# Optimization experiments

Measured on AMD Instinct MI355X. Metric: run time of the kernel, lower is better.

The kernel has to match this reference:

```python
import jax, jax.numpy as jnp
import numpy as np

HEADS = 8
DIM_HEAD = 64
WINDOW = 256
CAUSAL = True


def _sliding_window_mask(seq_len: int, window: int, causal: bool) -> jnp.ndarray:
    i = jnp.arange(seq_len)[:, None]
    j = jnp.arange(seq_len)[None, :]
    # attend iff i - window + 1 <= j <= i + window - 1 (end_pos exclusive)
    mask = (j >= i - window + 1) & (j <= i + window - 1)
    if causal:
        mask = mask & (j <= i)
    return mask  # (S, S) bool


def setup_inputs() -> dict:
    key = jax.random.key(0)
    k1, k2, k3 = jax.random.split(key, 3)
    dim = 512
    inner = HEADS * DIM_HEAD
    x = jax.random.normal(k1, (2, 2048, dim), dtype=jnp.float32)
    W_qkv = jax.random.normal(k2, (dim, 3 * inner), dtype=jnp.float32) * 0.02
    W_out = jax.random.normal(k3, (inner, dim), dtype=jnp.float32) * 0.02
    return {"x": x, "W_qkv": W_qkv, "W_out": W_out}


def reference(x, W_qkv, W_out):
    B, S, D = x.shape
    H, Dh = HEADS, DIM_HEAD
    scale = Dh ** (-0.5)
    qkv = x @ W_qkv  # (B, S, 3*H*Dh)
    q, k, v = jnp.split(qkv, 3, axis=-1)
    q = q.reshape(B, S, H, Dh).transpose(0, 2, 1, 3)  # (B, H, S, Dh)
    k = k.reshape(B, S, H, Dh).transpose(0, 2, 1, 3)
    v = v.reshape(B, S, H, Dh).transpose(0, 2, 1, 3)
    scores = jnp.einsum('bhid,bhjd->bhij', q, k) * scale
    mask = _sliding_window_mask(S, WINDOW, CAUSAL)
    mask_value = -jnp.finfo(scores.dtype).max
    scores = jnp.where(mask[None, None, :, :], scores, mask_value)
    attn = jax.nn.softmax(scores, axis=-1)  # (B, H, S, S)
    out = jnp.einsum('bhij,bhjd->bhid', attn, v)
    out = out.transpose(0, 2, 1, 3).reshape(B, S, H * Dh)
    out = out @ W_out  # (B, S, D)
    return (out, attn)
```

## Files before the change

### kernel.cpp

```cpp
#include <hip/hip_runtime.h>
#include <hip/hip_bf16.h>

typedef __bf16 bf16x8 __attribute__((ext_vector_type(8)));
typedef __bf16 bf16x4 __attribute__((ext_vector_type(4)));
typedef float f32x4 __attribute__((ext_vector_type(4)));

#define MFMA16(a,b,c) __builtin_amdgcn_mfma_f32_16x16x32_bf16(a, b, c, 0, 0, 0)

__global__ __launch_bounds__(256) void cvt_f32_bf16(const float* __restrict__ in,
                                                    __bf16* __restrict__ out, int n) {
  int i = (blockIdx.x * 256 + threadIdx.x) * 4;
  if (i >= n) return;
  float4 v = *reinterpret_cast<const float4*>(in + i);
  bf16x4 o;
  o[0] = (__bf16)v.x; o[1] = (__bf16)v.y; o[2] = (__bf16)v.z; o[3] = (__bf16)v.w;
  *reinterpret_cast<bf16x4*>(out + i) = o;
}

__global__ __launch_bounds__(256) void transpose_cvt(const float* __restrict__ in,
                                                     __bf16* __restrict__ out, int R, int C) {
  __shared__ float t[64][65];
  const int tilesC = C >> 6;
  const int tc = blockIdx.x % tilesC, tr = blockIdx.x / tilesC;
  const int r0 = tr << 6, c0 = tc << 6;
  const int tid = threadIdx.x;
  const int ri = tid >> 2, cq = (tid & 3) << 4;
#pragma unroll
  for (int e = 0; e < 16; e += 4) {
    float4 v = *reinterpret_cast<const float4*>(&in[(size_t)(r0 + ri) * C + c0 + cq + e]);
    t[ri][cq + e]     = v.x;
    t[ri][cq + e + 1] = v.y;
    t[ri][cq + e + 2] = v.z;
    t[ri][cq + e + 3] = v.w;
  }
  __syncthreads();
  const int co = tid >> 2, rq = (tid & 3) << 4;
  __attribute__((aligned(16))) __bf16 buf[16];
#pragma unroll
  for (int e = 0; e < 16; e++) buf[e] = (__bf16)t[rq + e][co];
  *reinterpret_cast<bf16x8*>(&out[(size_t)(c0 + co) * R + r0 + rq])     = *reinterpret_cast<bf16x8*>(&buf[0]);
  *reinterpret_cast<bf16x8*>(&out[(size_t)(c0 + co) * R + r0 + rq + 8]) = *reinterpret_cast<bf16x8*>(&buf[8]);
}

template <typename OT>
__global__ __launch_bounds__(256) void gemm_bt(const __bf16* __restrict__ A,
                                               const __bf16* __restrict__ Bt,
                                               OT* __restrict__ C, int M, int N, int K) {
  __shared__ __bf16 As[128][72];
  __shared__ __bf16 Bs[128][72];
  const int tid = threadIdx.x;
  const int wave = tid >> 6, lane = tid & 63;
  const int c = lane & 15, q4 = lane >> 4;
  const int bm = blockIdx.y << 7, bn = blockIdx.x << 7;
  const int wm = (wave >> 1) << 6, wn = (wave & 1) << 6;
  f32x4 acc[4][4];
#pragma unroll
  for (int m = 0; m < 4; m++)
#pragma unroll
    for (int n = 0; n < 4; n++)
#pragma unroll
      for (int e = 0; e < 4; e++) acc[m][n][e] = 0.f;

  const int srow = tid >> 1, scol = (tid & 1) << 5;
  for (int k0 = 0; k0 < K; k0 += 64) {
    __syncthreads();
    const __bf16* ag = A + (size_t)(bm + srow) * K + k0 + scol;
    const __bf16* bg = Bt + (size_t)(bn + srow) * K + k0 + scol;
    bf16x8 av[4], bv[4];
#pragma unroll
    for (int r = 0; r < 4; r++) av[r] = *reinterpret_cast<const bf16x8*>(ag + r * 8);
#pragma unroll
    for (int r = 0; r < 4; r++) bv[r] = *reinterpret_cast<const bf16x8*>(bg + r * 8);
#pragma unroll
    for (int r = 0; r < 4; r++) *reinterpret_cast<bf16x8*>(&As[srow][scol + r * 8]) = av[r];
#pragma unroll
    for (int r = 0; r < 4; r++) *reinterpret_cast<bf16x8*>(&Bs[srow][scol + r * 8]) = bv[r];
    __syncthreads();
#pragma unroll
    for (int ks = 0; ks < 2; ks++) {
      const int kk = ks * 32 + q4 * 8;
      bf16x8 af[4], bfv[4];
#pragma unroll
      for (int m = 0; m < 4; m++) af[m] = *reinterpret_cast<const bf16x8*>(&As[wm + m * 16 + c][kk]);
#pragma unroll
      for (int n = 0; n < 4; n++) bfv[n] = *reinterpret_cast<const bf16x8*>(&Bs[wn + n * 16 + c][kk]);
#pragma unroll
      for (int m = 0; m < 4; m++)
#pragma unroll
        for (int n = 0; n < 4; n++) acc[m][n] = MFMA16(af[m], bfv[n], acc[m][n]);
    }
  }
#pragma unroll
  for (int m = 0; m < 4; m++)
#pragma unroll
    for (int n = 0; n < 4; n++)
#pragma unroll
      for (int r2 = 0; r2 < 4; r2++) {
        const int row = bm + wm + m * 16 + q4 * 4 + r2;
        const int col = bn + wn + n * 16 + c;
        C[(size_t)row * N + col] = (OT)acc[m][n][r2];
      }
}

__global__ __launch_bounds__(256) void attn_fused(const __bf16* __restrict__ QKV,
                                                  float* __restrict__ attn,
                                                  __bf16* __restrict__ AO) {
  __shared__ __bf16 Qs[64][72];
  __shared__ __bf16 Ks[64][72];
  __shared__ __bf16 Ps[64][72];
  __shared__ float red[4][64];
  __shared__ float rowstat[64];
  const int qt = blockIdx.x, bh = blockIdx.y;
  const int b = bh >> 3, h = bh & 7;
  const int qi0 = qt << 6;
  const int tid = threadIdx.x;
  const int wave = tid >> 6, lane = tid & 63;
  const int c = lane & 15, q4 = lane >> 4;

  {
    const int r = tid >> 2, qq = (tid & 3) << 4;
    const __bf16* src = QKV + (size_t)(b * 2048 + qi0 + r) * 1536 + h * 64 + qq;
    bf16x8 v0 = *reinterpret_cast<const bf16x8*>(src);
    bf16x8 v1 = *reinterpret_cast<const bf16x8*>(src + 8);
    *reinterpret_cast<bf16x8*>(&Qs[r][qq]) = v0;
    *reinterpret_cast<bf16x8*>(&Qs[r][qq + 8]) = v1;
  }

  f32x4 acc[5][4];
#pragma unroll
  for (int t = 0; t < 5; t++)
#pragma unroll
    for (int m = 0; m < 4; m++)
#pragma unroll
      for (int e = 0; e < 4; e++) acc[t][m][e] = 0.f;

#pragma unroll
  for (int t = 0; t < 5; t++) {
    const int jt0 = (qt - 4 + t) << 6;
    if (jt0 < 0) continue;
    __syncthreads();
    {
      const int r = tid >> 2, qq = (tid & 3) << 4;
      const __bf16* src = QKV + (size_t)(b * 2048 + jt0 + r) * 1536 + 512 + h * 64 + qq;
      bf16x8 v0 = *reinterpret_cast<const bf16x8*>(src);
      bf16x8 v1 = *reinterpret_cast<const bf16x8*>(src + 8);
      *reinterpret_cast<bf16x8*>(&Ks[r][qq]) = v0;
      *reinterpret_cast<bf16x8*>(&Ks[r][qq + 8]) = v1;
    }
    __syncthreads();
#pragma unroll
    for (int ks = 0; ks < 2; ks++) {
      const int kk = ks * 32 + q4 * 8;
      bf16x8 bfr = *reinterpret_cast<const bf16x8*>(&Ks[wave * 16 + c][kk]);
#pragma unroll
      for (int m = 0; m < 4; m++) {
        bf16x8 afr = *reinterpret_cast<const bf16x8*>(&Qs[m * 16 + c][kk]);
        acc[t][m] = MFMA16(afr, bfr, acc[t][m]);
      }
    }
  }

  const float scale = 0.125f;
#pragma unroll
  for (int t = 0; t < 5; t++) {
    const int jb = ((qt - 4 + t) << 6) + wave * 16 + c;
#pragma unroll
    for (int m = 0; m < 4; m++)
#pragma unroll
      for (int r2 = 0; r2 < 4; r2++) {
        const int ig = qi0 + m * 16 + q4 * 4 + r2;
        const bool valid = (jb >= 0) && (jb <= ig) && (jb >= ig - 255);
        acc[t][m][r2] = valid ? acc[t][m][r2] * scale : -1e30f;
      }
  }

  float pm[16];
#pragma unroll
  for (int m = 0; m < 4; m++)
#pragma unroll
    for (int r2 = 0; r2 < 4; r2++) {
      float v = acc[0][m][r2];
#pragma unroll
      for (int t = 1; t < 5; t++) v = fmaxf(v, acc[t][m][r2]);
      pm[m * 4 + r2] = v;
    }
#pragma unroll
  for (int off = 8; off >= 1; off >>= 1)
#pragma unroll
    for (int i = 0; i < 16; i++) pm[i] = fmaxf(pm[i], __shfl_xor(pm[i], off, 64));
  if (c == 0) {
#pragma unroll
    for (int m = 0; m < 4; m++)
#pragma unroll
      for (int r2 = 0; r2 < 4; r2++) red[wave][m * 16 + q4 * 4 + r2] = pm[m * 4 + r2];
  }
  __syncthreads();
  if (tid < 64)
    rowstat[tid] = fmaxf(fmaxf(red[0][tid], red[1][tid]), fmaxf(red[2][tid], red[3][tid]));
  __syncthreads();

  float rmax[16], ps[16];
#pragma unroll
  for (int m = 0; m < 4; m++)
#pragma unroll
    for (int r2 = 0; r2 < 4; r2++) {
      rmax[m * 4 + r2] = rowstat[m * 16 + q4 * 4 + r2];
      ps[m * 4 + r2] = 0.f;
    }
#pragma unroll
  for (int t = 0; t < 5; t++)
#pragma unroll
    for (int m = 0; m < 4; m++)
#pragma unroll
      for (int r2 = 0; r2 < 4; r2++) {
        float p = __expf(acc[t][m][r2] - rmax[m * 4 + r2]);
        acc[t][m][r2] = p;
        ps[m * 4 + r2] += p;
      }
#pragma unroll
  for (int off = 8; off >= 1; off >>= 1)
#pragma unroll
    for (int i = 0; i < 16; i++) ps[i] += __shfl_xor(ps[i], off, 64);
  if (c == 0) {
#pragma unroll
    for (int m = 0; m < 4; m++)
#pragma unroll
      for (int r2 = 0; r2 < 4; r2++) red[wave][m * 16 + q4 * 4 + r2] = ps[m * 4 + r2];
  }
  __syncthreads();
  if (tid < 64) rowstat[tid] = red[0][tid] + red[1][tid] + red[2][tid] + red[3][tid];
  __syncthreads();

#pragma unroll
  for (int m = 0; m < 4; m++)
#pragma unroll
    for (int r2 = 0; r2 < 4; r2++) {
      const float rinv = 1.0f / rowstat[m * 16 + q4 * 4 + r2];
#pragma unroll
      for (int t = 0; t < 5; t++) acc[t][m][r2] *= rinv;
    }

  f32x4 o[4];
#pragma unroll
  for (int n = 0; n < 4; n++)
#pragma unroll
    for (int e = 0; e < 4; e++) o[n][e] = 0.f;

#pragma unroll
  for (int t = 0; t < 5; t++) {
    const int jt0 = (qt - 4 + t) << 6;
    if (jt0 < 0) continue;
    __syncthreads();
#pragma unroll
    for (int m = 0; m < 4; m++)
#pragma unroll
      for (int r2 = 0; r2 < 4; r2++)
        Ps[m * 16 + q4 * 4 + r2][wave * 16 + c] = (__bf16)acc[t][m][r2];
    {
      const int j = tid >> 2, dq = tid & 3;
#pragma unroll
      for (int r = 0; r < 2; r++) {
        const int d0 = (dq + r * 4) << 3;
        bf16x8 v = *reinterpret_cast<const bf16x8*>(
            QKV + (size_t)(b * 2048 + jt0 + j) * 1536 + 1024 + h * 64 + d0);
#pragma unroll
        for (int e = 0; e < 8; e++) Ks[d0 + e][j] = v[e];
      }
    }
    __syncthreads();
#pragma unroll
    for (int ks = 0; ks < 2; ks++) {
      const int kk = ks * 32 + q4 * 8;
      bf16x8 af = *reinterpret_cast<const bf16x8*>(&Ps[wave * 16 + c][kk]);
#pragma unroll
      for (int n = 0; n < 4; n++) {
        bf16x8 bfr = *reinterpret_cast<const bf16x8*>(&Ks[n * 16 + c][kk]);
        o[n] = MFMA16(af, bfr, o[n]);
      }
    }
  }

#pragma unroll
  for (int n = 0; n < 4; n++)
#pragma unroll
    for (int r2 = 0; r2 < 4; r2++) {
      const int i = qi0 + wave * 16 + q4 * 4 + r2;
      const int d = n * 16 + c;
      AO[(size_t)(b * 2048 + i) * 512 + h * 64 + d] = (__bf16)o[n][r2];
    }

  float* arow = attn + ((size_t)bh << 22);
#pragma unroll
  for (int t = 0; t < 5; t++) {
    const int jt0 = (qt - 4 + t) << 6;
    if (jt0 < 0) continue;
    const int jb = jt0 + wave * 16 + c;
#pragma unroll
    for (int m = 0; m < 4; m++)
#pragma unroll
      for (int r2 = 0; r2 < 4; r2++) {
        const int ig = qi0 + m * 16 + q4 * 4 + r2;
        arow[(size_t)ig * 2048 + jb] = acc[t][m][r2];
      }
  }

  const int bandLo = qt >= 4 ? ((qt - 4) << 6) : 0;
  const int bandHi = (qt + 1) << 6;
  const f32x4 z4 = {0.f, 0.f, 0.f, 0.f};
#pragma unroll 4
  for (int r = 0; r < 64; r++) {
    float* rp = arow + ((size_t)(qi0 + r) << 11);
#pragma unroll
    for (int pass = 0; pass < 2; pass++) {
      const int j = (pass << 10) + (tid << 2);
      if (j < bandLo || j >= bandHi)
        *reinterpret_cast<f32x4*>(rp + j) = z4;
    }
  }
}

extern "C" void kernel_launch(void* const* d_in, const int* in_sizes, int n_in,
                              void* d_out, int out_size, void* d_ws, size_t ws_size,
                              hipStream_t stream) {
  const float* x = (const float*)d_in[0];
  const float* Wqkv = (const float*)d_in[1];
  const float* Wout = (const float*)d_in[2];
  float* out = (float*)d_out;
  float* attn = out + (size_t)2 * 2048 * 512;

  char* ws = (char*)d_ws;
  __bf16* Xb   = (__bf16*)(ws);
  __bf16* Wqt  = (__bf16*)(ws + 4194304);
  __bf16* Wot  = (__bf16*)(ws + 4194304 + 1572864);
  __bf16* QKVb = (__bf16*)(ws + 4194304 + 1572864 + 524288);
  __bf16* AOb  = (__bf16*)(ws + 4194304 + 1572864 + 524288 + 12582912);

  cvt_f32_bf16<<<2048, 256, 0, stream>>>(x, Xb, 2 * 2048 * 512);
  transpose_cvt<<<192, 256, 0, stream>>>(Wqkv, Wqt, 512, 1536);
  transpose_cvt<<<64, 256, 0, stream>>>(Wout, Wot, 512, 512);

  gemm_bt<__bf16><<<dim3(12, 32), 256, 0, stream>>>(Xb, Wqt, QKVb, 4096, 1536, 512);

  attn_fused<<<dim3(32, 16), 256, 0, stream>>>(QKVb, attn, AOb);

  gemm_bt<float><<<dim3(4, 32), 256, 0, stream>>>(AOb, Wot, out, 4096, 512, 512);
}
```

Before: 100.3 us.

## Fuse prep kernels and move attn zero-fill into GEMM epilogues

The three conversion and transpose kernels are merged into one prep launch. Zero-filling the out-of-band attention entries moves from the attention kernel into the tails of the two GEMMs, split by row range (0-20000 in the QKV GEMM, the rest in the output GEMM), and now uses nontemporal stores. The goal is to cut launch count and spread the large, bandwidth-bound zero-fill across compute-bound GEMMs so the attention kernel only writes its band. The cost is extra tail work in the GEMMs, and the ordering relies on the fill regions never overlapping the band written by attention.

```diff
diff --git a/kernel.cpp b/kernel.cpp
--- a/kernel.cpp
+++ b/kernel.cpp
@@ -7,23 +7,27 @@
 
 #define MFMA16(a,b,c) __builtin_amdgcn_mfma_f32_16x16x32_bf16(a, b, c, 0, 0, 0)
 
-__global__ __launch_bounds__(256) void cvt_f32_bf16(const float* __restrict__ in,
-                                                    __bf16* __restrict__ out, int n) {
-  int i = (blockIdx.x * 256 + threadIdx.x) * 4;
-  if (i >= n) return;
-  float4 v = *reinterpret_cast<const float4*>(in + i);
-  bf16x4 o;
-  o[0] = (__bf16)v.x; o[1] = (__bf16)v.y; o[2] = (__bf16)v.z; o[3] = (__bf16)v.w;
-  *reinterpret_cast<bf16x4*>(out + i) = o;
-}
-
-__global__ __launch_bounds__(256) void transpose_cvt(const float* __restrict__ in,
-                                                     __bf16* __restrict__ out, int R, int C) {
-  __shared__ float t[64][65];
+__device__ inline void fill_attn_rows(float* __restrict__ attn, int rowStart, int rowEnd,
+                                      int tid) {
+  const f32x4 z4 = {0.f, 0.f, 0.f, 0.f};
+  for (int g = rowStart; g < rowEnd; g++) {
+    const int bh = g >> 11, i = g & 2047;
+    const int qt = i >> 6;
+    const int lo = qt >= 4 ? (qt - 4) << 6 : 0;
+    const int hi = (qt + 1) << 6;
+    float* rp = attn + ((size_t)bh << 22) + ((size_t)i << 11);
+    for (int j = tid << 2; j < lo; j += 1024)
+      __builtin_nontemporal_store(z4, reinterpret_cast<f32x4*>(rp + j));
+    for (int j = hi + (tid << 2); j < 2048; j += 1024)
+      __builtin_nontemporal_store(z4, reinterpret_cast<f32x4*>(rp + j));
+  }
+}
+
+__device__ inline void transpose_body(const float* __restrict__ in, __bf16* __restrict__ out,
+                                      int R, int C, int tile, int tid, float (*t)[65]) {
   const int tilesC = C >> 6;
-  const int tc = blockIdx.x % tilesC, tr = blockIdx.x / tilesC;
+  const int tc = tile % tilesC, tr = tile / tilesC;
   const int r0 = tr << 6, c0 = tc << 6;
-  const int tid = threadIdx.x;
   const int ri = tid >> 2, cq = (tid & 3) << 4;
 #pragma unroll
   for (int e = 0; e < 16; e += 4) {
@@ -42,10 +46,33 @@
   *reinterpret_cast<bf16x8*>(&out[(size_t)(c0 + co) * R + r0 + rq + 8]) = *reinterpret_cast<bf16x8*>(&buf[8]);
 }
 
+__global__ __launch_bounds__(256) void prep(const float* __restrict__ x,
+                                            const float* __restrict__ Wqkv,
+                                            const float* __restrict__ Wout,
+                                            __bf16* __restrict__ Xb,
+                                            __bf16* __restrict__ Wqt,
+                                            __bf16* __restrict__ Wot) {
+  __shared__ float t[64][65];
+  const int bid = blockIdx.x, tid = threadIdx.x;
+  if (bid < 2048) {
+    const int i = (bid * 256 + tid) * 4;
+    float4 v = *reinterpret_cast<const float4*>(x + i);
+    bf16x4 o;
+    o[0] = (__bf16)v.x; o[1] = (__bf16)v.y; o[2] = (__bf16)v.z; o[3] = (__bf16)v.w;
+    *reinterpret_cast<bf16x4*>(Xb + i) = o;
+  } else if (bid < 2240) {
+    transpose_body(Wqkv, Wqt, 512, 1536, bid - 2048, tid, t);
+  } else {
+    transpose_body(Wout, Wot, 512, 512, bid - 2240, tid, t);
+  }
+}
+
 template <typename OT>
 __global__ __launch_bounds__(256) void gemm_bt(const __bf16* __restrict__ A,
                                                const __bf16* __restrict__ Bt,
-                                               OT* __restrict__ C, int M, int N, int K) {
+                                               OT* __restrict__ C, int M, int N, int K,
+                                               float* __restrict__ fillAttn,
+                                               int fillStart, int fillEnd) {
   __shared__ __bf16 As[128][72];
   __shared__ __bf16 Bs[128][72];
   const int tid = threadIdx.x;
@@ -100,6 +127,15 @@
         const int col = bn + wn + n * 16 + c;
         C[(size_t)row * N + col] = (OT)acc[m][n][r2];
       }
+
+  const int nblocks = gridDim.x * gridDim.y;
+  const int bidLin = blockIdx.y * gridDim.x + blockIdx.x;
+  const int total = fillEnd - fillStart;
+  const int per = (total + nblocks - 1) / nblocks;
+  const int myStart = fillStart + bidLin * per;
+  int myEnd = myStart + per;
+  if (myEnd > fillEnd) myEnd = fillEnd;
+  if (myStart < myEnd) fill_attn_rows(fillAttn, myStart, myEnd, tid);
 }
 
 __global__ __launch_bounds__(256) void attn_fused(const __bf16* __restrict__ QKV,
@@ -303,20 +339,6 @@
         arow[(size_t)ig * 2048 + jb] = acc[t][m][r2];
       }
   }
-
-  const int bandLo = qt >= 4 ? ((qt - 4) << 6) : 0;
-  const int bandHi = (qt + 1) << 6;
-  const f32x4 z4 = {0.f, 0.f, 0.f, 0.f};
-#pragma unroll 4
-  for (int r = 0; r < 64; r++) {
-    float* rp = arow + ((size_t)(qi0 + r) << 11);
-#pragma unroll
-    for (int pass = 0; pass < 2; pass++) {
-      const int j = (pass << 10) + (tid << 2);
-      if (j < bandLo || j >= bandHi)
-        *reinterpret_cast<f32x4*>(rp + j) = z4;
-    }
-  }
 }
 
 extern "C" void kernel_launch(void* const* d_in, const int* in_sizes, int n_in,
@@ -335,13 +357,13 @@
   __bf16* QKVb = (__bf16*)(ws + 4194304 + 1572864 + 524288);
   __bf16* AOb  = (__bf16*)(ws + 4194304 + 1572864 + 524288 + 12582912);
 
-  cvt_f32_bf16<<<2048, 256, 0, stream>>>(x, Xb, 2 * 2048 * 512);
-  transpose_cvt<<<192, 256, 0, stream>>>(Wqkv, Wqt, 512, 1536);
-  transpose_cvt<<<64, 256, 0, stream>>>(Wout, Wot, 512, 512);
-
-  gemm_bt<__bf16><<<dim3(12, 32), 256, 0, stream>>>(Xb, Wqt, QKVb, 4096, 1536, 512);
+  prep<<<2304, 256, 0, stream>>>(x, Wqkv, Wout, Xb, Wqt, Wot);
+
+  gemm_bt<__bf16><<<dim3(12, 32), 256, 0, stream>>>(Xb, Wqt, QKVb, 4096, 1536, 512,
+                                                    attn, 0, 20000);
 
   attn_fused<<<dim3(32, 16), 256, 0, stream>>>(QKVb, attn, AOb);
 
-  gemm_bt<float><<<dim3(4, 32), 256, 0, stream>>>(AOb, Wot, out, 4096, 512, 512);
-}
+  gemm_bt<float><<<dim3(4, 32), 256, 0, stream>>>(AOb, Wot, out, 4096, 512, 512,
+                                                  attn, 20000, 32768);
+}
```

Result: slower. 109.2 us (+8.8%).
